# Performance work log

Measured on AMD Instinct MI355X. Metric: run time of the kernel, lower is better.

Reference implementation:

```python
import jax, jax.numpy as jnp
import numpy as np

G, L, K = 64, 256, 32          # graphs, residues per graph, max neighbors
N = G * L                       # 16384 nodes
HID = 32
NB = 10                         # number_of_basis
RADIUS = 5.0
C_S = float(np.sin(np.pi / 8.0))  # self-connection mixing (e3nn gate_points conv)
C_X = float(np.cos(np.pi / 8.0))
SQ3 = float(np.sqrt(3.0))         # l=1 SH 'component' normalization


def setup_inputs():
    rng = np.random.default_rng(0)
    # protein-like backbones: random walk with 3.8A steps per chain
    steps = rng.normal(size=(G, L, 3))
    steps /= np.linalg.norm(steps, axis=-1, keepdims=True)
    coords = np.cumsum(steps * 3.8, axis=1).reshape(N, 3).astype(np.float32)
    batch = np.repeat(np.arange(G, dtype=np.int32), L)
    # radius graph per chain, capped at K neighbors per destination, padded+masked
    c = coords.reshape(G, L, 3)
    d = np.linalg.norm(c[:, :, None, :] - c[:, None, :, :], axis=-1)
    d = d + np.eye(L, dtype=np.float32)[None] * 1e6   # exclude self loops
    idx = np.argsort(d, axis=-1)[:, :, :K]            # (G,L,K) nearest sources per dst
    dsel = np.take_along_axis(d, idx, axis=-1)
    valid = dsel < RADIUS
    off = (np.arange(G, dtype=np.int64) * L)[:, None, None]
    dst = np.broadcast_to(np.arange(N, dtype=np.int64).reshape(G, L, 1), (G, L, K))
    src = np.where(valid, idx.astype(np.int64) + off, dst)  # pad with self (masked)

    def w(k, shape):
        return jax.random.normal(jax.random.fold_in(jax.random.key(0), k), shape, dtype=jnp.float32)

    return dict(
        coords=jnp.asarray(coords),
        t=jax.random.uniform(jax.random.key(1), (G,), dtype=jnp.float32),
        batch=jnp.asarray(batch),
        edge_src=jnp.asarray(src.reshape(-1).astype(np.int32)),
        edge_dst=jnp.asarray(np.ascontiguousarray(dst).reshape(-1).astype(np.int32)),
        edge_mask=jnp.asarray(valid.reshape(-1).astype(np.float32)),
        sc1_w=w(1, (HID,)), lin1_w=w(2, (1,)),
        fc1_w0=w(3, (NB, HID)), fc1_w1=w(4, (HID, HID)), fc1_w2=w(5, (HID, 2)),
        conv1_l2s=w(6, (HID,)), conv1_l2v=w(7, (HID,)),
        sc2_w=w(8, (HID,)), lin1s_w=w(9, (HID, HID)), lin1v_w=w(10, (HID, HID)),
        fc2_w0=w(11, (NB, HID)), fc2_w1=w(12, (HID, HID)), fc2_w2=w(13, (HID, 2 * HID)),
        conv2_l2a=w(14, (HID,)), conv2_l2b=w(15, (HID,)),
    )


def _radial(emb, W0, W1, W2):
    # e3nn FullyConnectedNet: no bias, 1/sqrt(fan_in) weight scaling, SiLU hiddens
    h = jax.nn.silu(emb @ (W0 / np.sqrt(NB)))
    h = jax.nn.silu(h @ (W1 / np.sqrt(HID)))
    return h @ (W2 / np.sqrt(HID))


def reference(coords, t, batch, edge_src, edge_dst, edge_mask,
              sc1_w, lin1_w, fc1_w0, fc1_w1, fc1_w2, conv1_l2s, conv1_l2v,
              sc2_w, lin1s_w, lin1v_w, fc2_w0, fc2_w1, fc2_w2, conv2_l2a, conv2_l2b):
    n = coords.shape[0]
    a = t[batch]                                          # (N,) node_attr (0e scalar)
    vec = coords[edge_dst] - coords[edge_src]             # (E,3)
    r = jnp.sqrt(jnp.sum(vec * vec, axis=-1) + 1e-12)     # safe norm (padded self edges)
    sh1 = SQ3 * vec / r[:, None]                          # l=1 SH, component norm; sh0 == 1
    vals = jnp.linspace(0.0, RADIUS, NB)
    step = vals[1] - vals[0]
    emb = jnp.exp(-(((r[:, None] - vals) / step) ** 2)) / 1.12  # gaussian soft one-hot
    em = edge_mask                                        # (E,) 1=real edge, 0=padding
    inv_sqrt_k = 1.0 / np.sqrt(K)

    # ---- conv1: node input = 1x0e (ones) -> 32x0e + 32x1o ----
    sc_s = a[:, None] * sc1_w[None, :]                    # self-connection FCTP(0e,0e->32x0e)
    xp = a * lin1_w[0]                                    # lin1 FCTP(0e,0e->0e)
    w1 = _radial(emb, fc1_w0, fc1_w1, fc1_w2)             # (E,2) per-edge TP weights
    xs = xp[edge_src]
    mid_s = w1[:, 0] * xs * em                            # 0e x 0e -> 0e
    mid_v = (w1[:, 1] * xs * em)[:, None] * sh1           # 0e x 1o -> 1o
    nms = jax.ops.segment_sum(mid_s, edge_dst, num_segments=n) * inv_sqrt_k
    nmv = jax.ops.segment_sum(mid_v, edge_dst, num_segments=n) * inv_sqrt_k
    h_s = jax.nn.silu(C_S * sc_s + C_X * (nms * a)[:, None] * conv1_l2s[None, :])       # (N,32)
    h_v = jax.nn.silu(C_X * (nmv * a[:, None])[:, None, :] * conv1_l2v[None, :, None])  # (N,32,3) NB: elementwise SiLU as in source

    # ---- conv2: 32x0e+32x1o -> 1o ----
    sc_v = jnp.einsum('nuc,u->nc', h_v, sc2_w) * a[:, None] / np.sqrt(HID)  # self-connection
    s1 = (h_s @ (lin1s_w / np.sqrt(HID))) * a[:, None]
    v1 = jnp.einsum('nuc,uv->nvc', h_v, lin1v_w / np.sqrt(HID)) * a[:, None, None]
    w2 = _radial(emb, fc2_w0, fc2_w1, fc2_w2)             # (E,64) per-edge TP weights
    wa, wb = w2[:, :HID], w2[:, HID:]
    mid1 = (wa * s1[edge_src] * em[:, None])[:, :, None] * sh1[:, None, :]  # 0e x 1o -> 32x1o
    mid2 = v1[edge_src] * (wb * em[:, None])[:, :, None]                    # 1o x 0e -> 32x1o (sh0=1)
    m1 = jax.ops.segment_sum(mid1, edge_dst, num_segments=n) * inv_sqrt_k
    m2 = jax.ops.segment_sum(mid2, edge_dst, num_segments=n) * inv_sqrt_k
    conv_v = (jnp.einsum('nuc,u->nc', m1, conv2_l2a)
              + jnp.einsum('nuc,u->nc', m2, conv2_l2b)) * a[:, None] / np.sqrt(2 * HID)
    return C_S * sc_v + C_X * conv_v                      # (N,3) score vectors
```

## Files before the change

kernel.cpp:

```cpp
#include <hip/hip_runtime.h>

namespace {
constexpr int Kc = 32, HIDc = 32, NBc = 10;
constexpr float C_S = 0.3826834323650898f;
constexpr float C_X = 0.9238795325112867f;
constexpr float SQ3 = 1.7320508075688772f;
constexpr float INV_SQRT_K   = 0.17677669529663687f;
constexpr float INV_SQRT_HID = 0.17677669529663687f;
constexpr float INV_SQRT_NB  = 0.31622776601683794f;
constexpr float INV_SQRT_2HID = 0.125f;
constexpr float INV_STEP  = 1.8f;
constexpr float EMB_SCALE = 0.8928571428571429f;

typedef __attribute__((ext_vector_type(8)))  short bf16x8;
typedef __attribute__((ext_vector_type(16))) float f32x16;
typedef __attribute__((ext_vector_type(4)))  int   i32x4;

__device__ __forceinline__ float silu_div(float x) {
    return x / (1.0f + __expf(-x));
}
__device__ __forceinline__ float silu_rcp(float x) {
    return x * __builtin_amdgcn_rcpf(1.0f + __expf(-x));
}

__device__ __forceinline__ unsigned pk_hi(float a, float b) {
    unsigned ua = __builtin_bit_cast(unsigned, a);
    unsigned ub = __builtin_bit_cast(unsigned, b);
    return (ua >> 16) | (ub & 0xFFFF0000u);
}
__device__ __forceinline__ float trunc_hi(float a) {
    return __builtin_bit_cast(float, __builtin_bit_cast(unsigned, a) & 0xFFFF0000u);
}
__device__ __forceinline__ bf16x8 mk_frag(unsigned r0, unsigned r1, unsigned r2, unsigned r3) {
    i32x4 t; t[0] = (int)r0; t[1] = (int)r1; t[2] = (int)r2; t[3] = (int)r3;
    return __builtin_bit_cast(bf16x8, t);
}
__device__ __forceinline__ f32x16 mfma32(bf16x8 a, bf16x8 b, f32x16 c) {
    return __builtin_amdgcn_mfma_f32_32x32x16_bf16(a, b, c, 0, 0, 0);
}
}

__global__ __launch_bounds__(256) void se3_phase1(
    const float* __restrict__ coords, const float* __restrict__ t,
    const int* __restrict__ batch, const int* __restrict__ esrc,
    const float* __restrict__ emask,
    const float* __restrict__ sc1_w, const float* __restrict__ lin1_w,
    const float* __restrict__ W0, const float* __restrict__ W1,
    const float* __restrict__ W2,
    const float* __restrict__ l2s, const float* __restrict__ l2v,
    const float* __restrict__ sc2_w, const float* __restrict__ lin1s,
    const float* __restrict__ lin1v,
    const float* __restrict__ c2a, const float* __restrict__ c2b,
    const float* __restrict__ W2f2,
    float4* __restrict__ tab2, float* __restrict__ out_scpart)
{
    const int e    = blockIdx.x * 256 + threadIdx.x;
    const int n    = e >> 5;
    const int u    = threadIdx.x & 31;
    const int src  = esrc[e];
    const float em = emask[e];

    const float dx = coords[3 * n + 0] - coords[3 * src + 0];
    const float dy = coords[3 * n + 1] - coords[3 * src + 1];
    const float dz = coords[3 * n + 2] - coords[3 * src + 2];
    const float r  = sqrtf(dx * dx + dy * dy + dz * dz + 1e-12f);
    const float ir = 1.0f / r;
    const float shx = SQ3 * dx * ir, shy = SQ3 * dy * ir, shz = SQ3 * dz * ir;

    float emb[NBc];
#pragma unroll
    for (int b = 0; b < NBc; ++b) {
        const float d = r * INV_STEP - (float)b;
        emb[b] = __expf(-d * d) * EMB_SCALE;
    }

    float h1[HIDc];
#pragma unroll
    for (int j = 0; j < HIDc; ++j) {
        float acc = 0.f;
#pragma unroll
        for (int b = 0; b < NBc; ++b) acc = fmaf(emb[b], W0[b * HIDc + j], acc);
        h1[j] = silu_div(acc * INV_SQRT_NB);
    }

    float h2[HIDc];
#pragma unroll
    for (int j = 0; j < HIDc; ++j) {
        float acc = 0.f;
#pragma unroll
        for (int v = 0; v < HIDc; ++v) acc = fmaf(h1[v], W1[v * HIDc + j], acc);
        h2[j] = silu_div(acc * INV_SQRT_HID);
    }

    float w10 = 0.f, w11 = 0.f;
#pragma unroll
    for (int v = 0; v < HIDc; ++v) {
        w10 = fmaf(h2[v], W2[2 * v + 0], w10);
        w11 = fmaf(h2[v], W2[2 * v + 1], w11);
    }
    w10 *= INV_SQRT_HID;
    w11 *= INV_SQRT_HID;

    const float xs = t[batch[src]] * lin1_w[0];
    float ms = w10 * xs * em;
    const float fv = w11 * xs * em;
    float mvx = fv * shx, mvy = fv * shy, mvz = fv * shz;

#pragma unroll
    for (int m = 16; m >= 1; m >>= 1) {
        ms  += __shfl_xor(ms,  m, 32);
        mvx += __shfl_xor(mvx, m, 32);
        mvy += __shfl_xor(mvy, m, 32);
        mvz += __shfl_xor(mvz, m, 32);
    }
    const float nms = ms  * INV_SQRT_K;
    const float nvx = mvx * INV_SQRT_K;
    const float nvy = mvy * INV_SQRT_K;
    const float nvz = mvz * INV_SQRT_K;

    const float a  = t[batch[n]];
    const float hs = silu_div(C_S * a * sc1_w[u] + C_X * nms * a * l2s[u]);
    const float lv = l2v[u];
    const float hvx = silu_div(C_X * nvx * a * lv);
    const float hvy = silu_div(C_X * nvy * a * lv);
    const float hvz = silu_div(C_X * nvz * a * lv);

    const float s2 = sc2_w[u];
    float scx = hvx * s2, scy = hvy * s2, scz = hvz * s2;
#pragma unroll
    for (int m = 16; m >= 1; m >>= 1) {
        scx += __shfl_xor(scx, m, 32);
        scy += __shfl_xor(scy, m, 32);
        scz += __shfl_xor(scz, m, 32);
    }

    float s1 = 0.f, v1x = 0.f, v1y = 0.f, v1z = 0.f;
    for (int v = 0; v < HIDc; ++v) {
        const float hsv = __shfl(hs,  v, 32);
        const float hx  = __shfl(hvx, v, 32);
        const float hy  = __shfl(hvy, v, 32);
        const float hz  = __shfl(hvz, v, 32);
        const float wsv = lin1s[v * HIDc + u];
        const float wvv = lin1v[v * HIDc + u];
        s1  = fmaf(hsv, wsv, s1);
        v1x = fmaf(hx, wvv, v1x);
        v1y = fmaf(hy, wvv, v1y);
        v1z = fmaf(hz, wvv, v1z);
    }
    const float sa = INV_SQRT_HID * a;
    const float ox_ = s1  * sa * c2a[u];
    const float oy_ = v1x * sa * c2b[u];
    const float oz_ = v1y * sa * c2b[u];
    const float ow_ = v1z * sa * c2b[u];

    float A = 0.f, Bx = 0.f, By = 0.f, Bz = 0.f;
#pragma unroll
    for (int j = 0; j < HIDc; ++j) {
        const float ojx = __shfl(ox_, j, 32);
        const float ojy = __shfl(oy_, j, 32);
        const float ojz = __shfl(oz_, j, 32);
        const float ojw = __shfl(ow_, j, 32);
        const float wa  = W2f2[u * 64 + j];
        const float wb  = W2f2[u * 64 + 32 + j];
        A  = fmaf(wa, ojx, A);
        Bx = fmaf(wb, ojy, Bx);
        By = fmaf(wb, ojz, By);
        Bz = fmaf(wb, ojw, Bz);
    }
    float4 t2;
    t2.x = A  * INV_SQRT_HID;
    t2.y = Bx * INV_SQRT_HID;
    t2.z = By * INV_SQRT_HID;
    t2.w = Bz * INV_SQRT_HID;
    tab2[n * HIDc + u] = t2;

    if (u == 0) {
        const float s = C_S * a * INV_SQRT_HID;
        out_scpart[3 * n + 0] = scx * s;
        out_scpart[3 * n + 1] = scy * s;
        out_scpart[3 * n + 2] = scz * s;
    }
}

__global__ __launch_bounds__(256) void se3_phase2(
    const float* __restrict__ coords, const float* __restrict__ t,
    const int* __restrict__ esrc, const float* __restrict__ emask,
    const float* __restrict__ W0, const float* __restrict__ W1,
    const float4* __restrict__ tab2, float* __restrict__ out)
{
    const int lane = threadIdx.x & 63;
    const int col  = lane & 31;
    const int h    = lane >> 5;

    float a1v[8];
#pragma unroll
    for (int e2 = 0; e2 < 8; ++e2) {
        const int k = (e2 & 3) + 8 * (e2 >> 2) + 4 * h;
        a1v[e2] = (k < NBc) ? W0[k * HIDc + col] : 0.f;
    }
    unsigned a1h_[4], a1l_[4];
#pragma unroll
    for (int j = 0; j < 4; ++j) {
        const float x = a1v[2 * j], y = a1v[2 * j + 1];
        a1h_[j] = pk_hi(x, y);
        a1l_[j] = pk_hi(x - trunc_hi(x), y - trunc_hi(y));
    }
    const bf16x8 A1H = mk_frag(a1h_[0], a1h_[1], a1h_[2], a1h_[3]);
    const bf16x8 A1L = mk_frag(a1l_[0], a1l_[1], a1l_[2], a1l_[3]);

    bf16x8 A2H[2], A2L[2];
#pragma unroll
    for (int ks = 0; ks < 2; ++ks) {
        float w[8];
#pragma unroll
        for (int e2 = 0; e2 < 8; ++e2) {
            const int k = 16 * ks + (e2 & 3) + 8 * (e2 >> 2) + 4 * h;
            w[e2] = W1[k * HIDc + col];
        }
        unsigned rh[4], rl[4];
#pragma unroll
        for (int j = 0; j < 4; ++j) {
            rh[j] = pk_hi(w[2 * j], w[2 * j + 1]);
            rl[j] = pk_hi(w[2 * j] - trunc_hi(w[2 * j]),
                          w[2 * j + 1] - trunc_hi(w[2 * j + 1]));
        }
        A2H[ks] = mk_frag(rh[0], rh[1], rh[2], rh[3]);
        A2L[ks] = mk_frag(rl[0], rl[1], rl[2], rl[3]);
    }

    const int wid = blockIdx.x * 4 + (threadIdx.x >> 6);
    const int e0  = wid * 64;
    const int g   = e0 + lane;
    const int nA  = e0 >> 5;
    const int myn = g >> 5;
    const int src = esrc[g];
    const float em = emask[g];

    const float dx = coords[3 * myn + 0] - coords[3 * src + 0];
    const float dy = coords[3 * myn + 1] - coords[3 * src + 1];
    const float dz = coords[3 * myn + 2] - coords[3 * src + 2];
    const float r  = sqrtf(dx * dx + dy * dy + dz * dz + 1e-12f);
    const float ir = 1.0f / r;
    const float shx = SQ3 * dx * ir, shy = SQ3 * dy * ir, shz = SQ3 * dz * ir;

    float embv[NBc];
#pragma unroll
    for (int b = 0; b < NBc; ++b) {
        const float d = r * INV_STEP - (float)b;
        embv[b] = __expf(-d * d) * EMB_SCALE;
    }

    unsigned ph[5], pl[5];
#pragma unroll
    for (int j = 0; j < 5; ++j) {
        const float a0 = embv[2 * j], b0 = embv[2 * j + 1];
        ph[j] = pk_hi(a0, b0);
        pl[j] = pk_hi(a0 - trunc_hi(a0), b0 - trunc_hi(b0));
    }
    unsigned oph[5], opl[5];
#pragma unroll
    for (int j = 0; j < 5; ++j) {
        oph[j] = __shfl_xor(ph[j], 32, 64);
        opl[j] = __shfl_xor(pl[j], 32, 64);
    }

    const bf16x8 B1H0 = mk_frag(h ? oph[2] : ph[0], h ? oph[3] : ph[1], h ? 0u : ph[4], 0u);
    const bf16x8 B1L0 = mk_frag(h ? opl[2] : pl[0], h ? opl[3] : pl[1], h ? 0u : pl[4], 0u);
    const bf16x8 B1H1 = mk_frag(h ? ph[2] : oph[0], h ? ph[3] : oph[1], h ? 0u : oph[4], 0u);
    const bf16x8 B1L1 = mk_frag(h ? pl[2] : opl[0], h ? pl[3] : opl[1], h ? 0u : opl[4], 0u);

    float cxo[2], cyo[2], czo[2];

#pragma unroll
    for (int tI = 0; tI < 2; ++tI) {
        const bf16x8 B1H = tI ? B1H1 : B1H0;
        const bf16x8 B1L = tI ? B1L1 : B1L0;

        f32x16 c;
#pragma unroll
        for (int i = 0; i < 16; ++i) c[i] = 0.f;
        c = mfma32(A1H, B1H, c);
        c = mfma32(A1H, B1L, c);
        c = mfma32(A1L, B1H, c);
        c = mfma32(A1L, B1L, c);

        float h1v[16];
#pragma unroll
        for (int i = 0; i < 16; ++i) h1v[i] = silu_rcp(c[i] * INV_SQRT_NB);

        unsigned PH[8], PL[8];
#pragma unroll
        for (int i = 0; i < 8; ++i) {
            const float a0 = h1v[2 * i], b0 = h1v[2 * i + 1];
            PH[i] = pk_hi(a0, b0);
            PL[i] = pk_hi(a0 - trunc_hi(a0), b0 - trunc_hi(b0));
        }
        const bf16x8 B2H0 = mk_frag(PH[0], PH[1], PH[2], PH[3]);
        const bf16x8 B2L0 = mk_frag(PL[0], PL[1], PL[2], PL[3]);
        const bf16x8 B2H1 = mk_frag(PH[4], PH[5], PH[6], PH[7]);
        const bf16x8 B2L1 = mk_frag(PL[4], PL[5], PL[6], PL[7]);

        f32x16 c2;
#pragma unroll
        for (int i = 0; i < 16; ++i) c2[i] = 0.f;
        c2 = mfma32(A2H[0], B2H0, c2);
        c2 = mfma32(A2H[0], B2L0, c2);
        c2 = mfma32(A2L[0], B2H0, c2);
        c2 = mfma32(A2L[0], B2L0, c2);
        c2 = mfma32(A2H[1], B2H1, c2);
        c2 = mfma32(A2H[1], B2L1, c2);
        c2 = mfma32(A2L[1], B2H1, c2);
        c2 = mfma32(A2L[1], B2L1, c2);

        float h2v[16];
#pragma unroll
        for (int i = 0; i < 16; ++i) h2v[i] = silu_rcp(c2[i] * INV_SQRT_HID);

        const int   srcT = __shfl(src, tI * 32 + col, 64);
        const float emT  = __shfl(em,  tI * 32 + col, 64);
        const float sxT  = __shfl(shx, tI * 32 + col, 64);
        const float syT  = __shfl(shy, tI * 32 + col, 64);
        const float szT  = __shfl(shz, tI * 32 + col, 64);

        const float4* __restrict__ tp = tab2 + srcT * HIDc;
        float pp = 0.f, qx = 0.f, qy = 0.f, qz = 0.f;
#pragma unroll
        for (int i = 0; i < 16; ++i) {
            const int u2 = (i & 3) + 8 * (i >> 2) + 4 * h;
            const float4 gq = tp[u2];
            pp = fmaf(h2v[i], gq.x, pp);
            qx = fmaf(h2v[i], gq.y, qx);
            qy = fmaf(h2v[i], gq.z, qy);
            qz = fmaf(h2v[i], gq.w, qz);
        }
        pp += __shfl_xor(pp, 32, 64);
        qx += __shfl_xor(qx, 32, 64);
        qy += __shfl_xor(qy, 32, 64);
        qz += __shfl_xor(qz, 32, 64);

        float cx = emT * fmaf(pp, sxT, qx);
        float cy = emT * fmaf(pp, syT, qy);
        float cz = emT * fmaf(pp, szT, qz);
#pragma unroll
        for (int m = 16; m >= 1; m >>= 1) {
            cx += __shfl_xor(cx, m, 64);
            cy += __shfl_xor(cy, m, 64);
            cz += __shfl_xor(cz, m, 64);
        }
        cxo[tI] = cx; cyo[tI] = cy; czo[tI] = cz;
    }

    if (lane < 2) {
        const int n = nA + lane;
        const float a = t[n >> 8];
        const float s = C_X * a * INV_SQRT_2HID * INV_SQRT_K;
        const float vx = lane ? cxo[1] : cxo[0];
        const float vy = lane ? cyo[1] : cyo[0];
        const float vz = lane ? czo[1] : czo[0];
        out[3 * n + 0] += vx * s;
        out[3 * n + 1] += vy * s;
        out[3 * n + 2] += vz * s;
    }
}

extern "C" void kernel_launch(void* const* d_in, const int* in_sizes, int n_in,
                              void* d_out, int out_size, void* d_ws, size_t ws_size,
                              hipStream_t stream) {
    const float* coords = (const float*)d_in[0];
    const float* t      = (const float*)d_in[1];
    const int*   batch  = (const int*)d_in[2];
    const int*   esrc   = (const int*)d_in[3];
    const float* emask  = (const float*)d_in[5];
    const float* sc1_w  = (const float*)d_in[6];
    const float* lin1_w = (const float*)d_in[7];
    const float* fc1_w0 = (const float*)d_in[8];
    const float* fc1_w1 = (const float*)d_in[9];
    const float* fc1_w2 = (const float*)d_in[10];
    const float* c1l2s  = (const float*)d_in[11];
    const float* c1l2v  = (const float*)d_in[12];
    const float* sc2_w  = (const float*)d_in[13];
    const float* lin1s  = (const float*)d_in[14];
    const float* lin1v  = (const float*)d_in[15];
    const float* fc2_w0 = (const float*)d_in[16];
    const float* fc2_w1 = (const float*)d_in[17];
    const float* fc2_w2 = (const float*)d_in[18];
    const float* c2a    = (const float*)d_in[19];
    const float* c2b    = (const float*)d_in[20];

    float*  out  = (float*)d_out;
    float4* tab2 = (float4*)d_ws;

    const int nEdges = 16384 * Kc;
    dim3 block(256);
    dim3 grid(nEdges / 256);

    se3_phase1<<<grid, block, 0, stream>>>(coords, t, batch, esrc, emask,
        sc1_w, lin1_w, fc1_w0, fc1_w1, fc1_w2, c1l2s, c1l2v, sc2_w,
        lin1s, lin1v, c2a, c2b, fc2_w2, tab2, out);

    se3_phase2<<<grid, block, 0, stream>>>(coords, t, esrc, emask,
        fc2_w0, fc2_w1, tab2, out);
}
```

Baseline: 162.5 us.

## Compute conv1 radial MLP with split-bf16 MFMA instead of scalar FMAs

Phase 1's per-edge radial MLP (10->32->32->2), formerly per-thread scalar FMA loops, now runs as 32x32x16 bf16 MFMAs, one 32-edge tile per half-wave. Each fp32 operand is split into hi/lo bf16 parts and three or four cross products are accumulated to approximate fp32 accuracy. Weight fragments are built per thread at kernel start, and the emb vectors are exchanged between half-waves with shuffles. This cuts VALU work and register pressure from the 32-wide hidden arrays, at the cost of extra MFMA passes, fragment packing and small precision differences.

```diff
diff --git a/kernel.cpp b/kernel.cpp
--- a/kernel.cpp
+++ b/kernel.cpp
@@ -54,11 +54,61 @@
     const float* __restrict__ W2f2,
     float4* __restrict__ tab2, float* __restrict__ out_scpart)
 {
-    const int e    = blockIdx.x * 256 + threadIdx.x;
-    const int n    = e >> 5;
-    const int u    = threadIdx.x & 31;
-    const int src  = esrc[e];
-    const float em = emask[e];
+    const int lane = threadIdx.x & 63;
+    const int col  = lane & 31;
+    const int h    = lane >> 5;
+
+    float a1v[8];
+#pragma unroll
+    for (int e2 = 0; e2 < 8; ++e2) {
+        const int k = (e2 & 3) + 8 * (e2 >> 2) + 4 * h;
+        a1v[e2] = (k < NBc) ? W0[k * HIDc + col] : 0.f;
+    }
+    unsigned a1h_[4], a1l_[4];
+#pragma unroll
+    for (int j = 0; j < 4; ++j) {
+        const float x = a1v[2 * j], y = a1v[2 * j + 1];
+        a1h_[j] = pk_hi(x, y);
+        a1l_[j] = pk_hi(x - trunc_hi(x), y - trunc_hi(y));
+    }
+    const bf16x8 A1H = mk_frag(a1h_[0], a1h_[1], a1h_[2], a1h_[3]);
+    const bf16x8 A1L = mk_frag(a1l_[0], a1l_[1], a1l_[2], a1l_[3]);
+
+    bf16x8 A2H[2], A2L[2];
+#pragma unroll
+    for (int ks = 0; ks < 2; ++ks) {
+        float w[8];
+#pragma unroll
+        for (int e2 = 0; e2 < 8; ++e2) {
+            const int k = 16 * ks + (e2 & 3) + 8 * (e2 >> 2) + 4 * h;
+            w[e2] = W1[k * HIDc + col];
+        }
+        unsigned rh[4], rl[4];
+#pragma unroll
+        for (int j = 0; j < 4; ++j) {
+            rh[j] = pk_hi(w[2 * j], w[2 * j + 1]);
+            rl[j] = pk_hi(w[2 * j] - trunc_hi(w[2 * j]),
+                          w[2 * j + 1] - trunc_hi(w[2 * j + 1]));
+        }
+        A2H[ks] = mk_frag(rh[0], rh[1], rh[2], rh[3]);
+        A2L[ks] = mk_frag(rl[0], rl[1], rl[2], rl[3]);
+    }
+
+    float w2a[16], w2b[16];
+#pragma unroll
+    for (int i = 0; i < 16; ++i) {
+        const int u2 = (i & 3) + 8 * (i >> 2) + 4 * h;
+        w2a[i] = W2[2 * u2 + 0];
+        w2b[i] = W2[2 * u2 + 1];
+    }
+
+    const int wid = blockIdx.x * 4 + (threadIdx.x >> 6);
+    const int e0  = wid * 64;
+    const int g   = e0 + lane;
+    const int n   = g >> 5;
+    const int u   = col;
+    const int src = esrc[g];
+    const float em = emask[g];
 
     const float dx = coords[3 * n + 0] - coords[3 * src + 0];
     const float dy = coords[3 * n + 1] - coords[3 * src + 1];
@@ -67,39 +117,90 @@
     const float ir = 1.0f / r;
     const float shx = SQ3 * dx * ir, shy = SQ3 * dy * ir, shz = SQ3 * dz * ir;
 
-    float emb[NBc];
+    float embv[NBc];
 #pragma unroll
     for (int b = 0; b < NBc; ++b) {
         const float d = r * INV_STEP - (float)b;
-        emb[b] = __expf(-d * d) * EMB_SCALE;
-    }
-
-    float h1[HIDc];
-#pragma unroll
-    for (int j = 0; j < HIDc; ++j) {
-        float acc = 0.f;
-#pragma unroll
-        for (int b = 0; b < NBc; ++b) acc = fmaf(emb[b], W0[b * HIDc + j], acc);
-        h1[j] = silu_div(acc * INV_SQRT_NB);
-    }
-
-    float h2[HIDc];
-#pragma unroll
-    for (int j = 0; j < HIDc; ++j) {
-        float acc = 0.f;
-#pragma unroll
-        for (int v = 0; v < HIDc; ++v) acc = fmaf(h1[v], W1[v * HIDc + j], acc);
-        h2[j] = silu_div(acc * INV_SQRT_HID);
-    }
-
-    float w10 = 0.f, w11 = 0.f;
-#pragma unroll
-    for (int v = 0; v < HIDc; ++v) {
-        w10 = fmaf(h2[v], W2[2 * v + 0], w10);
-        w11 = fmaf(h2[v], W2[2 * v + 1], w11);
-    }
-    w10 *= INV_SQRT_HID;
-    w11 *= INV_SQRT_HID;
+        embv[b] = __expf(-d * d) * EMB_SCALE;
+    }
+
+    unsigned ph[5], pl[5];
+#pragma unroll
+    for (int j = 0; j < 5; ++j) {
+        const float a0 = embv[2 * j], b0 = embv[2 * j + 1];
+        ph[j] = pk_hi(a0, b0);
+        pl[j] = pk_hi(a0 - trunc_hi(a0), b0 - trunc_hi(b0));
+    }
+    unsigned oph[5], opl[5];
+#pragma unroll
+    for (int j = 0; j < 5; ++j) {
+        oph[j] = __shfl_xor(ph[j], 32, 64);
+        opl[j] = __shfl_xor(pl[j], 32, 64);
+    }
+
+    const bf16x8 B1H0 = mk_frag(h ? oph[2] : ph[0], h ? oph[3] : ph[1], h ? 0u : ph[4], 0u);
+    const bf16x8 B1L0 = mk_frag(h ? opl[2] : pl[0], h ? opl[3] : pl[1], h ? 0u : pl[4], 0u);
+    const bf16x8 B1H1 = mk_frag(h ? ph[2] : oph[0], h ? ph[3] : oph[1], h ? 0u : oph[4], 0u);
+    const bf16x8 B1L1 = mk_frag(h ? pl[2] : opl[0], h ? pl[3] : opl[1], h ? 0u : opl[4], 0u);
+
+    float w10t[2], w11t[2];
+
+#pragma unroll
+    for (int tI = 0; tI < 2; ++tI) {
+        const bf16x8 B1H = tI ? B1H1 : B1H0;
+        const bf16x8 B1L = tI ? B1L1 : B1L0;
+
+        f32x16 c;
+#pragma unroll
+        for (int i = 0; i < 16; ++i) c[i] = 0.f;
+        c = mfma32(A1H, B1H, c);
+        c = mfma32(A1H, B1L, c);
+        c = mfma32(A1L, B1H, c);
+        c = mfma32(A1L, B1L, c);
+
+        float h1v[16];
+#pragma unroll
+        for (int i = 0; i < 16; ++i) h1v[i] = silu_rcp(c[i] * INV_SQRT_NB);
+
+        unsigned PH[8], PL[8];
+#pragma unroll
+        for (int i = 0; i < 8; ++i) {
+            const float a0 = h1v[2 * i], b0 = h1v[2 * i + 1];
+            PH[i] = pk_hi(a0, b0);
+            PL[i] = pk_hi(a0 - trunc_hi(a0), b0 - trunc_hi(b0));
+        }
+        const bf16x8 B2H0 = mk_frag(PH[0], PH[1], PH[2], PH[3]);
+        const bf16x8 B2L0 = mk_frag(PL[0], PL[1], PL[2], PL[3]);
+        const bf16x8 B2H1 = mk_frag(PH[4], PH[5], PH[6], PH[7]);
+        const bf16x8 B2L1 = mk_frag(PL[4], PL[5], PL[6], PL[7]);
+
+        f32x16 c2;
+#pragma unroll
+        for (int i = 0; i < 16; ++i) c2[i] = 0.f;
+        c2 = mfma32(A2H[0], B2H0, c2);
+        c2 = mfma32(A2H[0], B2L0, c2);
+        c2 = mfma32(A2L[0], B2H0, c2);
+        c2 = mfma32(A2L[0], B2L0, c2);
+        c2 = mfma32(A2H[1], B2H1, c2);
+        c2 = mfma32(A2H[1], B2L1, c2);
+        c2 = mfma32(A2L[1], B2H1, c2);
+        c2 = mfma32(A2L[1], B2L1, c2);
+
+        float pw0 = 0.f, pw1 = 0.f;
+#pragma unroll
+        for (int i = 0; i < 16; ++i) {
+            const float h2i = silu_rcp(c2[i] * INV_SQRT_HID);
+            pw0 = fmaf(h2i, w2a[i], pw0);
+            pw1 = fmaf(h2i, w2b[i], pw1);
+        }
+        pw0 += __shfl_xor(pw0, 32, 64);
+        pw1 += __shfl_xor(pw1, 32, 64);
+        w10t[tI] = pw0;
+        w11t[tI] = pw1;
+    }
+
+    const float w10 = (h ? w10t[1] : w10t[0]) * INV_SQRT_HID;
+    const float w11 = (h ? w11t[1] : w11t[0]) * INV_SQRT_HID;
 
     const float xs = t[batch[src]] * lin1_w[0];
     float ms = w10 * xs * em;
```

Measured after the change: 151.7 us. 6.7% less time.
